# Performance work log

Measured on AMD Instinct MI355X. Metric: run time of the kernel, lower is better.

## Reference

```python
import jax, jax.numpy as jnp
import numpy as np

DIM = 768
N_HEADS = 12
HEAD_DIM = DIM // N_HEADS
MAX_REL = 3  # hardcoded in the module


def setup_inputs() -> dict:
    key = jax.random.key(0)
    ks = jax.random.split(key, 10)
    B, L = 4, 1024
    def xavier(k, shape):
        fan_in, fan_out = shape[-2], shape[-1]
        a = jnp.sqrt(6.0 / (fan_in + fan_out))
        return jax.random.uniform(k, shape, jnp.float32, -a, a)
    return {
        "query": jax.random.normal(ks[0], (B, L, DIM), jnp.float32),
        "key":   jax.random.normal(ks[1], (B, L, DIM), jnp.float32),
        "value": jax.random.normal(ks[2], (B, L, DIM), jnp.float32),
        "Wq": xavier(ks[3], (DIM, DIM)),
        "Wk": xavier(ks[4], (DIM, DIM)),
        "Wv": xavier(ks[5], (DIM, DIM)),
        "Wproj": xavier(ks[6], (DIM, DIM)),
        "b_proj": jnp.zeros((DIM,), jnp.float32),
        "rel_k_table": xavier(ks[7], (2 * MAX_REL + 1, HEAD_DIM)),
        "rel_v_table": xavier(ks[8], (2 * MAX_REL + 1, HEAD_DIM)),
    }


def _rel_embed(table, len_q, len_k):
    # [len_q, len_k, head_dim] gathered from clipped relative distances
    dist = jnp.arange(len_k)[None, :] - jnp.arange(len_q)[:, None]
    idx = jnp.clip(dist, -MAX_REL, MAX_REL) + MAX_REL
    return table[idx]


def reference(query, key, value, Wq, Wk, Wv, Wproj, b_proj, rel_k_table, rel_v_table):
    B, Lq, _ = query.shape
    Lk = key.shape[1]
    H, hd = N_HEADS, HEAD_DIM
    scale = hd ** (-0.5)

    q = query @ Wq.T                      # [B, Lq, D]
    k = key @ Wk.T                        # [B, Lk, D]
    v = value @ Wv.T                      # [B, Lk, D]

    qh = q.reshape(B, Lq, H, hd).transpose(0, 2, 1, 3)   # [B,H,Lq,hd]
    kh = k.reshape(B, Lk, H, hd).transpose(0, 2, 1, 3)
    vh = v.reshape(B, Lk, H, hd).transpose(0, 2, 1, 3)

    # content-content scores
    attn1 = jnp.einsum('bhqd,bhkd->bhqk', qh, kh)
    # content-relative-position scores
    rk = _rel_embed(rel_k_table, Lq, Lk)                  # [Lq,Lk,hd]
    attn2 = jnp.einsum('bhqd,qkd->bhqk', qh, rk)
    # NOTE: original code DIVIDES by scale (= hd**-0.5), i.e. multiplies by sqrt(hd)
    attn = (attn1 + attn2) / scale
    attn = jax.nn.softmax(attn, axis=-1)                  # [B,H,Lq,Lk]

    w1 = jnp.einsum('bhqk,bhkd->bhqd', attn, vh)
    rv = _rel_embed(rel_v_table, Lq, Lk)                  # [Lq,Lk,hd]
    w2 = jnp.einsum('bhqk,qkd->bhqd', attn, rv)

    x = (w1 + w2).transpose(0, 2, 1, 3).reshape(B, Lq, H * hd)
    x = x @ Wproj.T + b_proj
    return (x, attn)
```

## Files before the change

### kernel.cpp

```cpp
#include <hip/hip_runtime.h>

#define DIMM 768
#define NH 12
#define HD 64
#define LSEQ 1024
#define BATCH 4
#define NXE 3145728
#define NWE 589824

typedef __bf16 bf16x8 __attribute__((ext_vector_type(8)));
typedef float f32x4 __attribute__((ext_vector_type(4)));
typedef unsigned short u16;

static __device__ __forceinline__ u16 f2bf(float f) {
  unsigned u = __builtin_bit_cast(unsigned, f);
  u += 0x7fffu + ((u >> 16) & 1u);
  return (u16)(u >> 16);
}
static __device__ __forceinline__ float bf2f(u16 h) {
  unsigned u = ((unsigned)h) << 16;
  return __builtin_bit_cast(float, u);
}
static __device__ __forceinline__ bf16x8 ld8bf(const u16* p) {
  uint4 u = *(const uint4*)p;
  return __builtin_bit_cast(bf16x8, u);
}
#define MFMA(a, b, c) __builtin_amdgcn_mfma_f32_16x16x32_bf16(a, b, c, 0, 0, 0)
#define GLL(g, s)                                                      \
  __builtin_amdgcn_global_load_lds(                                    \
      (const __attribute__((address_space(1))) void*)(g),              \
      (__attribute__((address_space(3))) void*)(s), 16, 0, 0)

__global__ __launch_bounds__(256) void convert(
    const float* __restrict__ q_in, const float* __restrict__ k_in,
    const float* __restrict__ v_in, const float* __restrict__ Wq,
    const float* __restrict__ Wk, const float* __restrict__ Wv,
    const float* __restrict__ Wp, u16* __restrict__ AqH, u16* __restrict__ AqL,
    u16* __restrict__ AkH, u16* __restrict__ AkL, u16* __restrict__ Av,
    u16* __restrict__ WqH, u16* __restrict__ WqL, u16* __restrict__ WkH,
    u16* __restrict__ WkL, u16* __restrict__ Wvr, u16* __restrict__ Wpr) {
  long i = ((long)blockIdx.x * 256 + threadIdx.x) * 4;
  const float* src;
  u16 *dh, *dl = nullptr;
  long off;
  if (i < NXE) { src = q_in; dh = AqH; dl = AqL; off = i; }
  else if (i < 2L * NXE) { src = k_in; dh = AkH; dl = AkL; off = i - NXE; }
  else if (i < 3L * NXE) { src = v_in; dh = Av; off = i - 2L * NXE; }
  else {
    long j = i - 3L * NXE;
    int which = (int)(j / NWE);
    off = j % NWE;
    if (which == 0) { src = Wq; dh = WqH; dl = WqL; }
    else if (which == 1) { src = Wk; dh = WkH; dl = WkL; }
    else if (which == 2) { src = Wv; dh = Wvr; }
    else { src = Wp; dh = Wpr; }
  }
  float4 v = *(const float4*)(src + off);
  ushort4 h;
  h.x = f2bf(v.x); h.y = f2bf(v.y); h.z = f2bf(v.z); h.w = f2bf(v.w);
  *(ushort4*)(dh + off) = h;
  if (dl) {
    ushort4 lo;
    lo.x = f2bf(v.x - bf2f(h.x)); lo.y = f2bf(v.y - bf2f(h.y));
    lo.z = f2bf(v.z - bf2f(h.z)); lo.w = f2bf(v.w - bf2f(h.w));
    *(ushort4*)(dl + off) = lo;
  }
}

__global__ __launch_bounds__(256, 4) void gemm_multi(
    int mode0, const u16* __restrict__ AqH, const u16* __restrict__ AqL,
    const u16* __restrict__ AkH, const u16* __restrict__ AkL,
    const u16* __restrict__ Av, const u16* __restrict__ WqH,
    const u16* __restrict__ WqL, const u16* __restrict__ WkH,
    const u16* __restrict__ WkL, const u16* __restrict__ Wvr,
    const u16* __restrict__ Wpr, const u16* __restrict__ wbuf,
    u16* __restrict__ qhi, u16* __restrict__ qlo, u16* __restrict__ khi,
    u16* __restrict__ klo, u16* __restrict__ vT, float* __restrict__ outp,
    const float* __restrict__ bias) {
  __shared__ u16 sAh[64 * 32], sAl[64 * 32];
  __shared__ u16 sBh[128 * 32], sBl[128 * 32];
  const int mode = mode0 + blockIdx.z;
  const u16 *Ah, *Al = nullptr, *Bh, *Bl = nullptr;
  if (mode == 0) { Ah = AqH; Al = AqL; Bh = WqH; Bl = WqL; }
  else if (mode == 1) { Ah = AkH; Al = AkL; Bh = WkH; Bl = WkL; }
  else if (mode == 2) { Ah = Av; Bh = Wvr; }
  else { Ah = wbuf; Bh = Wpr; }
  const int t = threadIdx.x, w = t >> 6, l = t & 63;
  const int quad = l >> 4, l15 = l & 15;
  const int m0 = blockIdx.x * 64, n0 = blockIdx.y * 128;
  const int wm = (w & 1) * 32, wn = (w >> 1) * 64;
  const int srow = t >> 2, scol = (t & 3) * 8;
  const u16* gA = Ah + (m0 + srow) * DIMM + scol;
  const u16* gB = Bh + (n0 + srow) * DIMM + scol;
  const u16* gAl = (mode < 2) ? Al + (m0 + srow) * DIMM + scol : nullptr;
  const u16* gBl = (mode < 2) ? Bl + (n0 + srow) * DIMM + scol : nullptr;
  u16* lA = sAh + w * 512;
  u16* lB = sBh + w * 512;
  u16* lAl = sAl + w * 512;
  u16* lBl = sBl + w * 512;
  f32x4 acc[2][4] = {};

#define STAGE_G(k0)                                                    \
  do {                                                                 \
    GLL(gA + (k0), lA);                                                \
    GLL(gB + (k0), lB);                                                \
    GLL(gB + 64 * DIMM + (k0), lB + 2048);                             \
    if (mode < 2) {                                                    \
      GLL(gAl + (k0), lAl);                                            \
      GLL(gBl + (k0), lBl);                                            \
      GLL(gBl + 64 * DIMM + (k0), lBl + 2048);                         \
    }                                                                  \
  } while (0)

  STAGE_G(0);
  if (mode < 2) {
    for (int k0 = 0; k0 < DIMM; k0 += 32) {
      __syncthreads();
      bf16x8 ah[2], al[2], bh[4], bl[4];
#pragma unroll
      for (int i = 0; i < 2; ++i) {
        ah[i] = __builtin_bit_cast(
            bf16x8, *(const uint4*)(sAh + (wm + i * 16 + l15) * 32 + quad * 8));
        al[i] = __builtin_bit_cast(
            bf16x8, *(const uint4*)(sAl + (wm + i * 16 + l15) * 32 + quad * 8));
      }
#pragma unroll
      for (int j = 0; j < 4; ++j) {
        bh[j] = __builtin_bit_cast(
            bf16x8, *(const uint4*)(sBh + (wn + j * 16 + l15) * 32 + quad * 8));
        bl[j] = __builtin_bit_cast(
            bf16x8, *(const uint4*)(sBl + (wn + j * 16 + l15) * 32 + quad * 8));
      }
      __syncthreads();
      if (k0 + 32 < DIMM) STAGE_G(k0 + 32);
#pragma unroll
      for (int i = 0; i < 2; ++i)
#pragma unroll
        for (int j = 0; j < 4; ++j) acc[i][j] = MFMA(ah[i], bh[j], acc[i][j]);
#pragma unroll
      for (int i = 0; i < 2; ++i)
#pragma unroll
        for (int j = 0; j < 4; ++j) acc[i][j] = MFMA(al[i], bh[j], acc[i][j]);
#pragma unroll
      for (int i = 0; i < 2; ++i)
#pragma unroll
        for (int j = 0; j < 4; ++j) acc[i][j] = MFMA(ah[i], bl[j], acc[i][j]);
    }
  } else {
    for (int k0 = 0; k0 < DIMM; k0 += 32) {
      __syncthreads();
      bf16x8 ah[2], bh[4];
#pragma unroll
      for (int i = 0; i < 2; ++i)
        ah[i] = __builtin_bit_cast(
            bf16x8, *(const uint4*)(sAh + (wm + i * 16 + l15) * 32 + quad * 8));
#pragma unroll
      for (int j = 0; j < 4; ++j)
        bh[j] = __builtin_bit_cast(
            bf16x8, *(const uint4*)(sBh + (wn + j * 16 + l15) * 32 + quad * 8));
      __syncthreads();
      if (k0 + 32 < DIMM) STAGE_G(k0 + 32);
#pragma unroll
      for (int i = 0; i < 2; ++i)
#pragma unroll
        for (int j = 0; j < 4; ++j) acc[i][j] = MFMA(ah[i], bh[j], acc[i][j]);
    }
  }
#undef STAGE_G

  u16* oh = (mode == 0) ? qhi : khi;
  u16* ol = (mode == 0) ? qlo : klo;
#pragma unroll
  for (int i = 0; i < 2; ++i)
#pragma unroll
    for (int j = 0; j < 4; ++j)
#pragma unroll
      for (int r = 0; r < 4; ++r) {
        int grow = m0 + wm + i * 16 + quad * 4 + r;
        int gcol = n0 + wn + j * 16 + l15;
        float c = acc[i][j][r];
        int b = grow >> 10, ll = grow & 1023, h = gcol >> 6, d = gcol & 63;
        if (mode < 2) {
          int idx = ((b * NH + h) * LSEQ + ll) * HD + d;
          u16 hi = f2bf(c);
          oh[idx] = hi;
          ol[idx] = f2bf(c - bf2f(hi));
        } else if (mode == 2) {
          vT[((b * NH + h) * HD + d) * LSEQ + ll] = f2bf(c);
        } else {
          outp[grow * DIMM + gcol] = c + bias[gcol];
        }
      }
}

__global__ __launch_bounds__(256, 3) void attn_core(
    const u16* __restrict__ qhi, const u16* __restrict__ qlo,
    const u16* __restrict__ khi, const u16* __restrict__ klo,
    const u16* __restrict__ vT, const float* __restrict__ relk,
    const float* __restrict__ relv, float* __restrict__ attn_out,
    u16* __restrict__ wbuf) {
  __shared__ __align__(16) u16 uni[16 * 1032];
  __shared__ float qrel[16][7];
  __shared__ float arel[16][7];
  __shared__ float rvt[7][64];
  __shared__ float red[4][16][4];

  const int Lb = blockIdx.x + 64 * (blockIdx.y + NH * blockIdx.z);
  const int flat = (Lb & 7) * 384 + (Lb >> 3);
  const int qt = flat & 63, h = (flat >> 6) % NH, b = flat / (64 * NH);
  const int q0 = qt * 16;
  const int tid = threadIdx.x, wave = tid >> 6, lane = tid & 63;
  const int quad = lane >> 4, l15 = lane & 15;
  const int bhd = b * NH + h;

  const int rs = tid >> 3;
  const int cg = (tid & 7) ^ (rs & 7);
  const u16* gh = khi + (bhd * LSEQ + rs) * HD + cg * 8;
  const u16* gl = klo + (bhd * LSEQ + rs) * HD + cg * 8;
  u16* sb = uni + wave * 512;
  const int rowA = wave * 16 + l15;
  const int sw = rowA & 7;
  const int s0 = (rowA * 8 + (quad ^ sw)) * 8;
  const int s1 = (rowA * 8 + ((quad + 4) ^ sw)) * 8;

#define STAGE_K(c, bufsel)                                             \
  do {                                                                 \
    const u16* ghc_ = gh + (c) * (64 * HD);                            \
    const u16* glc_ = gl + (c) * (64 * HD);                            \
    u16* nb_ = sb + (bufsel) * 8192;                                   \
    GLL(ghc_, nb_);                                \
    GLL(ghc_ + 32 * HD, nb_ + 2048);               \
    GLL(glc_, nb_ + 4096);                         \
    GLL(glc_ + 32 * HD, nb_ + 6144);               \
  } while (0)

  STAGE_K(0, 0);

  for (int t = tid; t < 7 * HD; t += 256) rvt[t >> 6][t & 63] = relv[t];
  if (tid < 112) {
    int q = tid / 7, rr = tid % 7;
    const u16* qp = qhi + (bhd * LSEQ + q0 + q) * HD;
    const u16* lp = qlo + (bhd * LSEQ + q0 + q) * HD;
    const float* tp = relk + rr * HD;
    float s = 0.f;
#pragma unroll
    for (int d8 = 0; d8 < HD; d8 += 8) {
      uint4 uh = *(const uint4*)(qp + d8);
      uint4 ul = *(const uint4*)(lp + d8);
      float4 t0 = *(const float4*)(tp + d8);
      float4 t1 = *(const float4*)(tp + d8 + 4);
      unsigned hh[4] = {uh.x, uh.y, uh.z, uh.w};
      unsigned lv[4] = {ul.x, ul.y, ul.z, ul.w};
      float tv[8] = {t0.x, t0.y, t0.z, t0.w, t1.x, t1.y, t1.z, t1.w};
#pragma unroll
      for (int m = 0; m < 4; ++m) {
        s += (bf2f((u16)(hh[m] & 0xffff)) + bf2f((u16)(lv[m] & 0xffff))) * tv[2 * m];
        s += (bf2f((u16)(hh[m] >> 16)) + bf2f((u16)(lv[m] >> 16))) * tv[2 * m + 1];
      }
    }
    qrel[q][rr] = s;
    arel[q][rr] = 0.f;
  }

  f32x4 sc[16];
  {
    const int qbase = (bhd * LSEQ + q0 + l15) * HD + quad * 8;
    bf16x8 ah0 = ld8bf(qhi + qbase);
    bf16x8 ah1 = ld8bf(qhi + qbase + 32);
    bf16x8 al0 = ld8bf(qlo + qbase);
    bf16x8 al1 = ld8bf(qlo + qbase + 32);
    __syncthreads();
    for (int c = 0; c < 16; ++c) {
      if (c < 15) STAGE_K(c + 1, (c + 1) & 1);
      const u16* cur = uni + (c & 1) * 8192;
      bf16x8 kh0 = ld8bf(cur + s0);
      bf16x8 kh1 = ld8bf(cur + s1);
      bf16x8 kl0 = ld8bf(cur + 4096 + s0);
      bf16x8 kl1 = ld8bf(cur + 4096 + s1);
      f32x4 e = {}, f = {};
      e = MFMA(ah0, kh0, e);
      f = MFMA(ah1, kh1, f);
      e = MFMA(ah0, kl0, e);
      f = MFMA(ah1, kl1, f);
      e = MFMA(al0, kh0, e);
      f = MFMA(al1, kh1, f);
      sc[c] = e + f;
      __syncthreads();
    }
  }

  const int colbase = wave * 16 + l15;
  const int dbase = colbase - q0 - quad * 4;
  float mrow[4] = {-3.4e38f, -3.4e38f, -3.4e38f, -3.4e38f};
#pragma unroll
  for (int c = 0; c < 16; ++c)
#pragma unroll
    for (int r = 0; r < 4; ++r) {
      int d = dbase + c * 64 - r;
      int ri = d < -3 ? 0 : (d > 3 ? 6 : d + 3);
      float s = (sc[c][r] + qrel[quad * 4 + r][ri]) * 8.0f;
      sc[c][r] = s;
      mrow[r] = fmaxf(mrow[r], s);
    }
#pragma unroll
  for (int m = 1; m <= 8; m <<= 1)
#pragma unroll
    for (int r = 0; r < 4; ++r) mrow[r] = fmaxf(mrow[r], __shfl_xor(mrow[r], m));
  if (l15 < 4) {
    float mv = l15 == 0 ? mrow[0] : l15 == 1 ? mrow[1] : l15 == 2 ? mrow[2] : mrow[3];
    red[0][quad * 4 + l15][wave] = mv;
  }
  __syncthreads();
  float mx[4];
#pragma unroll
  for (int r = 0; r < 4; ++r) {
    int row = quad * 4 + r;
    mx[r] = fmaxf(fmaxf(red[0][row][0], red[0][row][1]),
                  fmaxf(red[0][row][2], red[0][row][3]));
  }

  float sum[4] = {}, s0a[4] = {}, s6a[4] = {};
#pragma unroll
  for (int c = 0; c < 16; ++c)
#pragma unroll
    for (int r = 0; r < 4; ++r) {
      float e = __expf(sc[c][r] - mx[r]);
      sc[c][r] = e;
      int d = dbase + c * 64 - r;
      sum[r] += e;
      if (d <= -3) s0a[r] += e;
      if (d >= 3) s6a[r] += e;
    }
#pragma unroll
  for (int m = 1; m <= 8; m <<= 1)
#pragma unroll
    for (int r = 0; r < 4; ++r) {
      sum[r] += __shfl_xor(sum[r], m);
      s0a[r] += __shfl_xor(s0a[r], m);
      s6a[r] += __shfl_xor(s6a[r], m);
    }
  if (l15 < 4) {
    int row = quad * 4 + l15;
    float sv = l15 == 0 ? sum[0] : l15 == 1 ? sum[1] : l15 == 2 ? sum[2] : sum[3];
    float a0 = l15 == 0 ? s0a[0] : l15 == 1 ? s0a[1] : l15 == 2 ? s0a[2] : s0a[3];
    float a6 = l15 == 0 ? s6a[0] : l15 == 1 ? s6a[1] : l15 == 2 ? s6a[2] : s6a[3];
    red[1][row][wave] = sv;
    red[2][row][wave] = a0;
    red[3][row][wave] = a6;
  }
  __syncthreads();
  float rn[4];
#pragma unroll
  for (int r = 0; r < 4; ++r) {
    int row = quad * 4 + r;
    float s = red[1][row][0] + red[1][row][1] + red[1][row][2] + red[1][row][3];
    rn[r] = 1.0f / s;
    if (wave == 0 && l15 == 0) {
      float t0 = red[2][row][0] + red[2][row][1] + red[2][row][2] + red[2][row][3];
      float t6 = red[3][row][0] + red[3][row][1] + red[3][row][2] + red[3][row][3];
      arel[row][0] = t0 * rn[r];
      arel[row][6] = t6 * rn[r];
    }
  }

#pragma unroll
  for (int c = 0; c < 16; ++c) {
    int col = colbase + c * 64;
#pragma unroll
    for (int r = 0; r < 4; ++r) {
      int row = quad * 4 + r;
      float p = sc[c][r] * rn[r];
      uni[row * 1032 + col] = f2bf(p);
      int d = dbase + c * 64 - r;
      if (d >= -2 && d <= 2) arel[row][d + 3] = p;
    }
  }
  __syncthreads();

  {
    float* aob = attn_out + ((size_t)(bhd * LSEQ + q0)) * LSEQ;
#pragma unroll
    for (int row = 0; row < 16; ++row) {
      uint2 u = *(const uint2*)&uni[row * 1032 + tid * 4];
      float4 f = {bf2f((u16)(u.x & 0xffff)), bf2f((u16)(u.x >> 16)),
                  bf2f((u16)(u.y & 0xffff)), bf2f((u16)(u.y >> 16))};
      *(float4*)(aob + row * LSEQ + tid * 4) = f;
    }
  }

  {
    const u16* vb = vT + (bhd * HD + wave * 16 + l15) * LSEQ;
    f32x4 acc0 = {}, acc1 = {};
#pragma unroll 4
    for (int kk = 0; kk < LSEQ; kk += 64) {
      int ak = kk + quad * 8;
      bf16x8 aP0 = __builtin_bit_cast(bf16x8, *(const uint4*)&uni[l15 * 1032 + ak]);
      bf16x8 bV0 = ld8bf(vb + ak);
      acc0 = MFMA(aP0, bV0, acc0);
      bf16x8 aP1 = __builtin_bit_cast(bf16x8, *(const uint4*)&uni[l15 * 1032 + ak + 32]);
      bf16x8 bV1 = ld8bf(vb + ak + 32);
      acc1 = MFMA(aP1, bV1, acc1);
    }
    f32x4 acc = acc0 + acc1;
    const int col = wave * 16 + l15;
#pragma unroll
    for (int r = 0; r < 4; ++r) {
      int row = quad * 4 + r;
      float w2 = 0.f;
#pragma unroll
      for (int t = 0; t < 7; ++t) w2 += arel[row][t] * rvt[t][col];
      wbuf[(b * LSEQ + q0 + row) * DIMM + h * HD + col] = f2bf(acc[r] + w2);
    }
  }
#undef STAGE_K
}

extern "C" void kernel_launch(void* const* d_in, const int* in_sizes, int n_in,
                              void* d_out, int out_size, void* d_ws, size_t ws_size,
                              hipStream_t stream) {
  const float* q_in = (const float*)d_in[0];
  const float* k_in = (const float*)d_in[1];
  const float* v_in = (const float*)d_in[2];
  const float* Wq = (const float*)d_in[3];
  const float* Wk = (const float*)d_in[4];
  const float* Wv = (const float*)d_in[5];
  const float* Wp = (const float*)d_in[6];
  const float* bias = (const float*)d_in[7];
  const float* relk = (const float*)d_in[8];
  const float* relv = (const float*)d_in[9];
  float* out = (float*)d_out;

  u16* p = (u16*)d_ws;
  u16 *AqH = p, *AqL = AqH + NXE, *AkH = AqL + NXE, *AkL = AkH + NXE,
      *Av = AkL + NXE;
  u16 *WqH = Av + NXE, *WqL = WqH + NWE, *WkH = WqL + NWE, *WkL = WkH + NWE,
      *Wvr = WkL + NWE, *Wpr = Wvr + NWE;
  u16 *qhi = Wpr + NWE, *qlo = qhi + NXE, *khi = qlo + NXE, *klo = khi + NXE,
      *vT = klo + NXE, *wbuf = vT + NXE;

  convert<<<(3 * NXE + 4 * NWE) / 1024, 256, 0, stream>>>(
      q_in, k_in, v_in, Wq, Wk, Wv, Wp, AqH, AqL, AkH, AkL, Av, WqH, WqL, WkH,
      WkL, Wvr, Wpr);
  gemm_multi<<<dim3(64, 6, 3), 256, 0, stream>>>(
      0, AqH, AqL, AkH, AkL, Av, WqH, WqL, WkH, WkL, Wvr, Wpr, wbuf, qhi, qlo,
      khi, klo, vT, out, bias);
  attn_core<<<dim3(64, NH, BATCH), 256, 0, stream>>>(
      qhi, qlo, khi, klo, vT, relk, relv, out + NXE, wbuf);
  gemm_multi<<<dim3(64, 6, 1), 256, 0, stream>>>(
      3, AqH, AqL, AkH, AkL, Av, WqH, WqL, WkH, WkL, Wvr, Wpr, wbuf, qhi, qlo,
      khi, klo, vT, out, bias);
}
```

Before: 439.6 us.

## Replace global-to-LDS K staging with register-prefetched double buffer

The K-tile staging in the score loop no longer uses direct global-to-LDS loads. It now prefetches two chunks ahead into registers, writes them to the alternate LDS buffer after the MFMAs, and synchronises with explicit waitcnt and barrier instructions in a fully unrolled loop. The aim is to hide global load latency behind compute and drop one full __syncthreads per iteration. In exchange it uses more VGPRs for the staged uint4 values, which could lower occupancy, and it relies on the barrier and swizzle layout matching the old scheme.

Result: faster. 430.0 us (-2.2%).

```diff
diff --git a/kernel.cpp b/kernel.cpp
--- a/kernel.cpp
+++ b/kernel.cpp
@@ -217,24 +217,51 @@
   const int cg = (tid & 7) ^ (rs & 7);
   const u16* gh = khi + (bhd * LSEQ + rs) * HD + cg * 8;
   const u16* gl = klo + (bhd * LSEQ + rs) * HD + cg * 8;
-  u16* sb = uni + wave * 512;
+  u16* const wslot = uni + tid * 8;
   const int rowA = wave * 16 + l15;
   const int sw = rowA & 7;
   const int s0 = (rowA * 8 + (quad ^ sw)) * 8;
   const int s1 = (rowA * 8 + ((quad + 4) ^ sw)) * 8;
 
-#define STAGE_K(c, bufsel)                                             \
-  do {                                                                 \
-    const u16* ghc_ = gh + (c) * (64 * HD);                            \
-    const u16* glc_ = gl + (c) * (64 * HD);                            \
-    u16* nb_ = sb + (bufsel) * 8192;                                   \
-    GLL(ghc_, nb_);                                \
-    GLL(ghc_ + 32 * HD, nb_ + 2048);               \
-    GLL(glc_, nb_ + 4096);                         \
-    GLL(glc_ + 32 * HD, nb_ + 6144);               \
+  uint4 sA0, sA1, sA2, sA3, sB0, sB1, sB2, sB3;
+#define LOADA(c)                                                     \
+  do {                                                               \
+    sA0 = *(const uint4*)(gh + (c) * (64 * HD));                     \
+    sA1 = *(const uint4*)(gh + (c) * (64 * HD) + 32 * HD);           \
+    sA2 = *(const uint4*)(gl + (c) * (64 * HD));                     \
+    sA3 = *(const uint4*)(gl + (c) * (64 * HD) + 32 * HD);           \
   } while (0)
-
-  STAGE_K(0, 0);
+#define LOADB(c)                                                     \
+  do {                                                               \
+    sB0 = *(const uint4*)(gh + (c) * (64 * HD));                     \
+    sB1 = *(const uint4*)(gh + (c) * (64 * HD) + 32 * HD);           \
+    sB2 = *(const uint4*)(gl + (c) * (64 * HD));                     \
+    sB3 = *(const uint4*)(gl + (c) * (64 * HD) + 32 * HD);           \
+  } while (0)
+#define DSWRITE_A(bufsel)                                            \
+  do {                                                               \
+    u16* d_ = wslot + (bufsel) * 8192;                               \
+    *(uint4*)(d_) = sA0;                                             \
+    *(uint4*)(d_ + 2048) = sA1;                                      \
+    *(uint4*)(d_ + 4096) = sA2;                                      \
+    *(uint4*)(d_ + 6144) = sA3;                                      \
+  } while (0)
+#define DSWRITE_B(bufsel)                                            \
+  do {                                                               \
+    u16* d_ = wslot + (bufsel) * 8192;                               \
+    *(uint4*)(d_) = sB0;                                             \
+    *(uint4*)(d_ + 2048) = sB1;                                      \
+    *(uint4*)(d_ + 4096) = sB2;                                      \
+    *(uint4*)(d_ + 6144) = sB3;                                      \
+  } while (0)
+
+  const int qbase = (bhd * LSEQ + q0 + l15) * HD + quad * 8;
+  bf16x8 ah0 = ld8bf(qhi + qbase);
+  bf16x8 ah1 = ld8bf(qhi + qbase + 32);
+  bf16x8 al0 = ld8bf(qlo + qbase);
+  bf16x8 al1 = ld8bf(qlo + qbase + 32);
+  LOADA(0);
+  LOADB(1);
 
   for (int t = tid; t < 7 * HD; t += 256) rvt[t >> 6][t & 63] = relv[t];
   if (tid < 112) {
@@ -262,32 +289,41 @@
     arel[q][rr] = 0.f;
   }
 
+  DSWRITE_A(0);
+  asm volatile("s_waitcnt lgkmcnt(0)" ::: "memory");
+  __builtin_amdgcn_sched_barrier(0);
+  __builtin_amdgcn_s_barrier();
+
   f32x4 sc[16];
-  {
-    const int qbase = (bhd * LSEQ + q0 + l15) * HD + quad * 8;
-    bf16x8 ah0 = ld8bf(qhi + qbase);
-    bf16x8 ah1 = ld8bf(qhi + qbase + 32);
-    bf16x8 al0 = ld8bf(qlo + qbase);
-    bf16x8 al1 = ld8bf(qlo + qbase + 32);
-    __syncthreads();
-    for (int c = 0; c < 16; ++c) {
-      if (c < 15) STAGE_K(c + 1, (c + 1) & 1);
-      const u16* cur = uni + (c & 1) * 8192;
-      bf16x8 kh0 = ld8bf(cur + s0);
-      bf16x8 kh1 = ld8bf(cur + s1);
-      bf16x8 kl0 = ld8bf(cur + 4096 + s0);
-      bf16x8 kl1 = ld8bf(cur + 4096 + s1);
-      f32x4 e = {}, f = {};
-      e = MFMA(ah0, kh0, e);
-      f = MFMA(ah1, kh1, f);
-      e = MFMA(ah0, kl0, e);
-      f = MFMA(ah1, kl1, f);
-      e = MFMA(al0, kh0, e);
-      f = MFMA(al1, kh1, f);
-      sc[c] = e + f;
-      __syncthreads();
-    }
-  }
+#pragma unroll
+  for (int c = 0; c < 16; ++c) {
+    const u16* cur = uni + (c & 1) * 8192;
+    bf16x8 kh0 = ld8bf(cur + s0);
+    bf16x8 kh1 = ld8bf(cur + s1);
+    bf16x8 kl0 = ld8bf(cur + 4096 + s0);
+    bf16x8 kl1 = ld8bf(cur + 4096 + s1);
+    f32x4 e = {}, f = {};
+    e = MFMA(ah0, kh0, e);
+    f = MFMA(ah1, kh1, f);
+    e = MFMA(ah0, kl0, e);
+    f = MFMA(ah1, kl1, f);
+    e = MFMA(al0, kh0, e);
+    f = MFMA(al1, kh1, f);
+    sc[c] = e + f;
+    if (c < 14) {
+      if ((c & 1) == 0) LOADA(c + 2); else LOADB(c + 2);
+    }
+    if (c < 15) {
+      if ((c & 1) == 0) DSWRITE_B(1); else DSWRITE_A(0);
+      asm volatile("s_waitcnt lgkmcnt(0)" ::: "memory");
+      __builtin_amdgcn_sched_barrier(0);
+      __builtin_amdgcn_s_barrier();
+    }
+  }
+#undef LOADA
+#undef LOADB
+#undef DSWRITE_A
+#undef DSWRITE_B
 
   const int colbase = wave * 16 + l15;
   const int dbase = colbase - q0 - quad * 4;
@@ -412,7 +448,6 @@
       wbuf[(b * LSEQ + q0 + row) * DIMM + h * HD + col] = f2bf(acc[r] + w2);
     }
   }
-#undef STAGE_K
 }
 
 extern "C" void kernel_launch(void* const* d_in, const int* in_sizes, int n_in,
```
